# Performance work log

Hardware: AMD Instinct MI355X
Metric: run time of the kernel (lower is better)

## Reference

```python
import jax, jax.numpy as jnp
import numpy as np

N_NODES = 100000
DROPOUT_P = 0.2


def _gcn_conv(x, W, b, src, dst, n_nodes):
    # PyG GCNConv: h = x @ W; add self-loops; sym-norm deg^-1/2 aggregation; + bias
    h = x @ W  # [N, D_out]
    loops = jnp.arange(n_nodes, dtype=src.dtype)
    src_all = jnp.concatenate([src, loops])
    dst_all = jnp.concatenate([dst, loops])
    deg = jax.ops.segment_sum(jnp.ones_like(dst_all, dtype=h.dtype), dst_all,
                              num_segments=n_nodes)  # includes self-loops
    dinv = jnp.where(deg > 0, jax.lax.rsqrt(deg), 0.0)
    norm = dinv[src_all] * dinv[dst_all]  # [E+N]
    msg = h[src_all] * norm[:, None]      # gather + scale
    out = jax.ops.segment_sum(msg, dst_all, num_segments=n_nodes)  # scatter-add
    return out + b


def setup_inputs() -> dict:
    key = jax.random.key(0)
    k1, k2, k3, k4 = jax.random.split(key, 4)
    x = jax.random.normal(k1, (N_NODES, 128), dtype=jnp.float32)
    edge_index = jax.random.randint(k2, (2, 1600000), 0, N_NODES, dtype=jnp.int64)
    W1 = jax.random.normal(k3, (128, 64), dtype=jnp.float32) * (1.0 / np.sqrt(128))
    b1 = jnp.zeros((64,), dtype=jnp.float32)
    W2 = jax.random.normal(k4, (64, 32), dtype=jnp.float32) * (1.0 / np.sqrt(64))
    b2 = jnp.zeros((32,), dtype=jnp.float32)
    return {"x": x, "edge_index": edge_index, "W1": W1, "b1": b1, "W2": W2, "b2": b2}


def reference(x, edge_index, W1, b1, W2, b2):
    src, dst = edge_index[0], edge_index[1]
    h1 = _gcn_conv(x, W1, b1, src, dst, N_NODES)
    h1 = jax.nn.relu(h1)
    # F.dropout defaults to training=True -> apply inverted dropout with fixed key
    keep = jax.random.bernoulli(jax.random.key(42), 1.0 - DROPOUT_P, h1.shape)
    h1 = jnp.where(keep, h1 / (1.0 - DROPOUT_P), 0.0)
    h2 = _gcn_conv(h1, W2, b2, src, dst, N_NODES)
    return h2
```

## Files before the change

### kernel.cpp

```cpp
#include <hip/hip_runtime.h>
#include <stdint.h>

#define DIN 128
#define D1 64
#define D2 32
#define MAXDEG 48
#define BCAP 4608
#define BINBLK 4096
#define NBKPAD 512

__device__ __forceinline__ unsigned short f2bf(float v) {
  unsigned u = __float_as_uint(v);
  unsigned r = u + 0x7fffu + ((u >> 16) & 1u);
  return (unsigned short)(r >> 16);
}
__device__ __forceinline__ float bflo(unsigned u) { return __uint_as_float(u << 16); }
__device__ __forceinline__ float bfhi(unsigned u) { return __uint_as_float(u & 0xffff0000u); }

__device__ __forceinline__ unsigned rotl32(unsigned x, int r) {
  return (x << r) | (x >> (32 - r));
}

__device__ __forceinline__ unsigned threefry_fold(unsigned ctr) {
  unsigned k0 = 0u, k1 = 42u;
  unsigned ks0 = k0, ks1 = k1, ks2 = k0 ^ k1 ^ 0x1BD11BDAu;
  unsigned x0 = 0u, x1 = ctr;
  x0 += ks0; x1 += ks1;
#define TF_ROUND(r) { x0 += x1; x1 = rotl32(x1, (r)); x1 ^= x0; }
  TF_ROUND(13) TF_ROUND(15) TF_ROUND(26) TF_ROUND(6)
  x0 += ks1; x1 += ks2 + 1u;
  TF_ROUND(17) TF_ROUND(29) TF_ROUND(16) TF_ROUND(24)
  x0 += ks2; x1 += ks0 + 2u;
  TF_ROUND(13) TF_ROUND(15) TF_ROUND(26) TF_ROUND(6)
  x0 += ks0; x1 += ks1 + 3u;
  TF_ROUND(17) TF_ROUND(29) TF_ROUND(16) TF_ROUND(24)
  x0 += ks1; x1 += ks2 + 4u;
  TF_ROUND(13) TF_ROUND(15) TF_ROUND(26) TF_ROUND(6)
  x0 += ks2; x1 += ks0 + 5u;
#undef TF_ROUND
  return x0 ^ x1;
}

__device__ __forceinline__ float dropout_scale(unsigned idx) {
  unsigned bits = threefry_fold(idx);
  float u = __uint_as_float((bits >> 9) | 0x3f800000u) - 1.0f;
  return (u < 0.8f) ? 1.25f : 0.0f;
}

__device__ __forceinline__ uint4 grow64(const unsigned short* p, int s, int fc) {
  return *(const uint4*)((const char*)p + (((unsigned)s << 7) + ((unsigned)fc << 1)));
}
__device__ __forceinline__ uint4 grow32(const unsigned short* p, int s, int fc) {
  return *(const uint4*)((const char*)p + (((unsigned)s << 6) + ((unsigned)fc << 1)));
}

__device__ __forceinline__ void addpk(float2& a, unsigned u) {
  a.x += bflo(u);
  a.y += bfhi(u);
}
__device__ __forceinline__ void addpkm(float2& a, unsigned u, float m) {
  a.x = fmaf(m, bflo(u), a.x);
  a.y = fmaf(m, bfhi(u), a.y);
}

template <int K>
__device__ __forceinline__ void gather_acc1(float2 (&acc)[4], int sv, float dvv, int cnt,
                                            int d, int fc,
                                            const unsigned short* __restrict__ h1p, int eslot) {
  uint4 v[K];
  float dv[K];
#pragma unroll
  for (int seg = 0; seg < K - 1; seg++) {
    int e = seg * 8 + eslot;
    int s = __shfl(sv, e, 64);
    dv[seg] = __shfl(dvv, e, 64);
    v[seg] = grow64(h1p, s, fc);
  }
  {
    const int elast = (K - 1) * 8 + eslot;
    const bool ok = elast < cnt;
    int s = __shfl(sv, elast, 64);
    float dl = __shfl(dvv, elast, 64);
    dv[K - 1] = ok ? dl : 0.0f;
    v[K - 1] = grow64(h1p, ok ? s : d, fc);
  }
#pragma unroll
  for (int seg = 0; seg < K; seg++) {
    addpkm(acc[0], v[seg].x, dv[seg]); addpkm(acc[1], v[seg].y, dv[seg]);
    addpkm(acc[2], v[seg].z, dv[seg]); addpkm(acc[3], v[seg].w, dv[seg]);
  }
}

template <int K>
__device__ __forceinline__ void gather_acc2(float2 (&acc)[4], int sv, int cnt, int d, int fc,
                                            const unsigned short* __restrict__ h2p, int eslot) {
  uint4 v[K];
#pragma unroll
  for (int seg = 0; seg < K - 1; seg++) {
    int s = __shfl(sv, seg * 16 + eslot, 64);
    v[seg] = grow32(h2p, s, fc);
  }
  const int elast = (K - 1) * 16 + eslot;
  const bool ok = elast < cnt;
  {
    int s = __shfl(sv, elast, 64);
    v[K - 1] = grow32(h2p, ok ? s : d, fc);
  }
#pragma unroll
  for (int seg = 0; seg < K - 1; seg++) {
    addpk(acc[0], v[seg].x); addpk(acc[1], v[seg].y);
    addpk(acc[2], v[seg].z); addpk(acc[3], v[seg].w);
  }
  const float m = ok ? 1.0f : 0.0f;
  addpkm(acc[0], v[K - 1].x, m); addpkm(acc[1], v[K - 1].y, m);
  addpkm(acc[2], v[K - 1].z, m); addpkm(acc[3], v[K - 1].w, m);
}

struct BinShared {
  int cnt[NBKPAD];
  int cbase[NBKPAD];
};
struct G1Shared {
  float xT[32][65];
  float Wl[32][D1];
};
union K1Shared {
  BinShared bin;
  G1Shared g1;
};

__global__ __launch_bounds__(256) void fused1_kernel(const int* __restrict__ src,
                                                     const int* __restrict__ dst,
                                                     int* __restrict__ cursor,
                                                     unsigned* __restrict__ binned,
                                                     int E, int NBK, int nbin,
                                                     const float* __restrict__ x,
                                                     const float* __restrict__ W1,
                                                     unsigned short* __restrict__ h1p, int N) {
  __shared__ K1Shared sh;
  const int tid = threadIdx.x;

  if ((int)blockIdx.x < nbin) {
    const int e0 = blockIdx.x * BINBLK;
    const bool full = (e0 + BINBLK) <= E;

    for (int b = tid; b < NBKPAD; b += 256) sh.bin.cnt[b] = 0;
    __syncthreads();

    int dreg[16];
    if (full) {
#pragma unroll
      for (int i = 0; i < 4; i++) {
        int4 q = *(const int4*)(dst + e0 + 4 * tid + 1024 * i);
        dreg[4 * i + 0] = q.x; dreg[4 * i + 1] = q.y;
        dreg[4 * i + 2] = q.z; dreg[4 * i + 3] = q.w;
      }
    } else {
#pragma unroll
      for (int i = 0; i < 16; i++) {
        int e = e0 + 4 * tid + 1024 * (i >> 2) + (i & 3);
        dreg[i] = (e < E) ? dst[e] : -1;
      }
    }
#pragma unroll
    for (int i = 0; i < 16; i++)
      if (dreg[i] >= 0) atomicAdd(&sh.bin.cnt[dreg[i] >> 8], 1);
    __syncthreads();

    for (int b = tid; b < NBK; b += 256) {
      int c = sh.bin.cnt[b];
      if (c > 0) sh.bin.cbase[b] = b * BCAP + atomicAdd(&cursor[b], c);
      sh.bin.cnt[b] = 0;
    }
    __syncthreads();

    int sreg[16];
    if (full) {
#pragma unroll
      for (int i = 0; i < 4; i++) {
        int4 q = *(const int4*)(src + e0 + 4 * tid + 1024 * i);
        sreg[4 * i + 0] = q.x; sreg[4 * i + 1] = q.y;
        sreg[4 * i + 2] = q.z; sreg[4 * i + 3] = q.w;
      }
    } else {
#pragma unroll
      for (int i = 0; i < 16; i++) {
        int e = e0 + 4 * tid + 1024 * (i >> 2) + (i & 3);
        sreg[i] = (e < E) ? src[e] : 0;
      }
    }
#pragma unroll
    for (int i = 0; i < 16; i++) {
      int d = dreg[i];
      if (d >= 0) {
        int b = d >> 8;
        int rk = atomicAdd(&sh.bin.cnt[b], 1);
        int pos = sh.bin.cbase[b] + rk;
        if (pos - b * BCAP < BCAP)
          binned[pos] = ((unsigned)(d & 255) << 24) | (unsigned)sreg[i];
      }
    }
  } else {
    const int rowbase = ((int)blockIdx.x - nbin) * 64;
    const int tx = tid & 15;
    const int ty = tid >> 4;
    float acc[4][4];
#pragma unroll
    for (int i = 0; i < 4; i++)
#pragma unroll
      for (int j = 0; j < 4; j++) acc[i][j] = 0.f;

    for (int c4 = 0; c4 < 4; c4++) {
      const int k0 = c4 * 32;
#pragma unroll
      for (int i = 0; i < 2; i++) {
        int f = tid + 256 * i;
        int row = f >> 3;
        int kq = (f & 7) * 4;
        int gr = rowbase + row;
        float4 vv = make_float4(0.f, 0.f, 0.f, 0.f);
        if (gr < N) vv = *(const float4*)(x + (size_t)gr * DIN + k0 + kq);
        sh.g1.xT[kq + 0][row] = vv.x;
        sh.g1.xT[kq + 1][row] = vv.y;
        sh.g1.xT[kq + 2][row] = vv.z;
        sh.g1.xT[kq + 3][row] = vv.w;
      }
#pragma unroll
      for (int i = 0; i < 2; i++) {
        int f = tid + 256 * i;
        int k = f >> 4;
        int cc = (f & 15) * 4;
        *(float4*)&sh.g1.Wl[k][cc] = *(const float4*)(W1 + (size_t)(k0 + k) * D1 + cc);
      }
      __syncthreads();
#pragma unroll 4
      for (int k = 0; k < 32; k++) {
        float4 a = *(const float4*)&sh.g1.xT[k][4 * ty];
        float4 b = *(const float4*)&sh.g1.Wl[k][4 * tx];
        float av[4] = {a.x, a.y, a.z, a.w};
        float bv[4] = {b.x, b.y, b.z, b.w};
#pragma unroll
        for (int i = 0; i < 4; i++)
#pragma unroll
          for (int j = 0; j < 4; j++) acc[i][j] = fmaf(av[i], bv[j], acc[i][j]);
      }
      __syncthreads();
    }

#pragma unroll
    for (int i = 0; i < 4; i++) {
      int gr = rowbase + 4 * ty + i;
      if (gr < N) {
        ushort4 o;
        o.x = f2bf(acc[i][0]);
        o.y = f2bf(acc[i][1]);
        o.z = f2bf(acc[i][2]);
        o.w = f2bf(acc[i][3]);
        *(ushort4*)(h1p + (size_t)gr * D1 + 4 * tx) = o;
      }
    }
  }
}

__global__ __launch_bounds__(256) void ellbuild_kernel(const unsigned* __restrict__ binned,
                                                       const int* __restrict__ cursor,
                                                       int* __restrict__ deg,
                                                       float* __restrict__ dinv,
                                                       int* __restrict__ ell, int N) {
  __shared__ int r[256];
  __shared__ int ellw[256 * MAXDEG];
  const int tid = threadIdx.x;
  const int b = blockIdx.x;
  const int nodebase = b << 8;
  r[tid] = 0;
  __syncthreads();

  int cnt = cursor[b];
  if (cnt > BCAP) cnt = BCAP;
  const unsigned* seg = binned + (size_t)b * BCAP;
  for (int i = tid; i < cnt; i += 256) {
    unsigned p = seg[i];
    int local = (int)(p >> 24);
    int rk = atomicAdd(&r[local], 1);
    if (rk < MAXDEG) ellw[local * MAXDEG + rk] = (int)(p & 0x00FFFFFFu);
  }
  __syncthreads();

  int4* dst4 = (int4*)(ell + (size_t)nodebase * MAXDEG);
  const int4* src4 = (const int4*)ellw;
#pragma unroll
  for (int i = 0; i < (256 * MAXDEG / 4) / 256; i++)
    dst4[tid + 256 * i] = src4[tid + 256 * i];

  int node = nodebase + tid;
  if (node < N) {
    int dg = r[tid];
    deg[node] = dg;
    dinv[node] = (float)(1.0 / sqrt((double)(dg + 1)));
  }
}

__global__ __launch_bounds__(256) void agg1_kernel(const int* __restrict__ deg,
                                                   const float* __restrict__ dinv,
                                                   const int* __restrict__ ell,
                                                   const unsigned short* __restrict__ h1p,
                                                   const float* __restrict__ b1,
                                                   const float* __restrict__ W2,
                                                   unsigned short* __restrict__ h2p, int N) {
  __shared__ float red[4][528];
  __shared__ float W2l[D1 * D2];
  const int tid = threadIdx.x;
  const int wslot = __builtin_amdgcn_readfirstlane(tid >> 6);
  const int d = blockIdx.x * 4 + wslot;
  const int lane = tid & 63;
  const int eslot = lane >> 3;
  const int fc = (lane & 7) << 3;
  const int f = fc + eslot;
  const int c = lane & 31;
  const int h = lane >> 5;
  const int cnt = min(deg[d], MAXDEG);
  const int base = d * MAXDEG;

  {
    float4* w4 = (float4*)W2l;
    const float4* g4 = (const float4*)W2;
    w4[tid] = g4[tid];
    w4[tid + 256] = g4[tid + 256];
  }

  int sv = ell[base + lane];
  sv = (lane < cnt) ? sv : d;
  float dvv = dinv[sv];
  uint4 self = grow64(h1p, d, fc);
  const float di = dinv[d];
  const float bias = b1[f];
  const float drop = dropout_scale((unsigned)(d * D1 + f));

  __syncthreads();

  float2 acc[4];
  {
    float m = (eslot == 0) ? di : 0.0f;
    acc[0] = make_float2(m * bflo(self.x), m * bfhi(self.x));
    acc[1] = make_float2(m * bflo(self.y), m * bfhi(self.y));
    acc[2] = make_float2(m * bflo(self.z), m * bfhi(self.z));
    acc[3] = make_float2(m * bflo(self.w), m * bfhi(self.w));
  }

  switch ((cnt + 7) >> 3) {
    case 6: gather_acc1<6>(acc, sv, dvv, cnt, d, fc, h1p, eslot); break;
    case 5: gather_acc1<5>(acc, sv, dvv, cnt, d, fc, h1p, eslot); break;
    case 4: gather_acc1<4>(acc, sv, dvv, cnt, d, fc, h1p, eslot); break;
    case 3: gather_acc1<3>(acc, sv, dvv, cnt, d, fc, h1p, eslot); break;
    case 2: gather_acc1<2>(acc, sv, dvv, cnt, d, fc, h1p, eslot); break;
    case 1: gather_acc1<1>(acc, sv, dvv, cnt, d, fc, h1p, eslot); break;
    default: break;
  }

  float* wred = red[wslot];
  *(float4*)&wred[eslot * 66 + fc]     = make_float4(acc[0].x, acc[0].y, acc[1].x, acc[1].y);
  *(float4*)&wred[eslot * 66 + fc + 4] = make_float4(acc[2].x, acc[2].y, acc[3].x, acc[3].y);
  float vsum = 0.f;
#pragma unroll
  for (int e = 0; e < 8; e++) vsum += wred[e * 66 + f];

  float o = fmaf(di, vsum, bias);
  o = fmaxf(o, 0.0f);
  o *= drop;

  wred[f] = o;
  const float* w2h = &W2l[(h * 32) * D2 + c];
  float p = 0.f;
#pragma unroll
  for (int i = 0; i < 8; i++) {
    float4 hv = *(const float4*)&wred[h * 32 + 4 * i];
    p = fmaf(hv.x, w2h[(4 * i + 0) * D2], p);
    p = fmaf(hv.y, w2h[(4 * i + 1) * D2], p);
    p = fmaf(hv.z, w2h[(4 * i + 2) * D2], p);
    p = fmaf(hv.w, w2h[(4 * i + 3) * D2], p);
  }
  p += __shfl_down(p, 32, 64);
  if (h == 0) h2p[(size_t)d * D2 + c] = f2bf(di * p);
}

__global__ __launch_bounds__(256) void agg2_kernel(const int* __restrict__ deg,
                                                   const float* __restrict__ dinv,
                                                   const int* __restrict__ ell,
                                                   const unsigned short* __restrict__ h2p,
                                                   const float* __restrict__ b2,
                                                   float* __restrict__ out, int N) {
  __shared__ float red[4][544];
  const int wslot = __builtin_amdgcn_readfirstlane(threadIdx.x >> 6);
  const int d = blockIdx.x * 4 + wslot;
  const int lane = threadIdx.x & 63;
  const int eslot = lane >> 2;
  const int fc = (lane & 3) << 3;
  const int cnt = min(deg[d], MAXDEG);
  const int base = d * MAXDEG;

  int sv = ell[base + lane];
  uint4 self = grow32(h2p, d, fc);
  const float di = dinv[d];

  float2 acc[4];
  {
    float m = (eslot == 0) ? 1.0f : 0.0f;
    acc[0] = make_float2(m * bflo(self.x), m * bfhi(self.x));
    acc[1] = make_float2(m * bflo(self.y), m * bfhi(self.y));
    acc[2] = make_float2(m * bflo(self.z), m * bfhi(self.z));
    acc[3] = make_float2(m * bflo(self.w), m * bfhi(self.w));
  }

  switch ((cnt + 15) >> 4) {
    case 3: gather_acc2<3>(acc, sv, cnt, d, fc, h2p, eslot); break;
    case 2: gather_acc2<2>(acc, sv, cnt, d, fc, h2p, eslot); break;
    case 1: gather_acc2<1>(acc, sv, cnt, d, fc, h2p, eslot); break;
    default: break;
  }

  float* wred = red[wslot];
  *(float4*)&wred[eslot * 34 + fc]     = make_float4(acc[0].x, acc[0].y, acc[1].x, acc[1].y);
  *(float4*)&wred[eslot * 34 + fc + 4] = make_float4(acc[2].x, acc[2].y, acc[3].x, acc[3].y);
  const int f = fc + (eslot & 7);
  const int ebase = (lane >= 32) ? 8 : 0;
  float vsum = 0.f;
#pragma unroll
  for (int e = 0; e < 8; e++) vsum += wred[(ebase + e) * 34 + f];
  vsum += __shfl_down(vsum, 32, 64);

  if (lane < 32) {
    out[(size_t)d * D2 + f] = fmaf(di, vsum, b2[f]);
  }
}

extern "C" void kernel_launch(void* const* d_in, const int* in_sizes, int n_in,
                              void* d_out, int out_size, void* d_ws, size_t ws_size,
                              hipStream_t stream) {
  const float* x  = (const float*)d_in[0];
  const int*   ei = (const int*)d_in[1];
  const float* W1 = (const float*)d_in[2];
  const float* b1 = (const float*)d_in[3];
  const float* W2 = (const float*)d_in[4];
  const float* b2 = (const float*)d_in[5];
  const int N = in_sizes[0] / DIN;
  const int E = in_sizes[1] / 2;
  const int NBK = (N + 255) >> 8;
  const int* src = ei;
  const int* dst = ei + E;
  float* out = (float*)d_out;

  char* ws = (char*)d_ws;
  size_t off = 0;
  auto alloc = [&](size_t bytes) -> char* {
    char* p = ws + off;
    off += (bytes + 255) / 256 * 256;
    return p;
  };
  unsigned short* h1p = (unsigned short*)alloc((size_t)N * D1 * 2);
  unsigned short* h2p = (unsigned short*)alloc((size_t)N * D2 * 2);
  char*       scratch = alloc((size_t)NBK * BCAP * 4);
  int*            ell = (int*)alloc(((size_t)NBK * 256 * MAXDEG + 64) * 4);
  int*            deg = (int*)alloc((size_t)N * 4);
  float*        dinvp = (float*)alloc((size_t)N * 4);
  int*         cursor = (int*)alloc((size_t)NBK * 4);
  unsigned*    binned = (unsigned*)scratch;
  (void)ws_size; (void)n_in; (void)out_size;

  hipMemsetAsync(cursor, 0, (size_t)NBK * 4, stream);

  const int NB_BIN = (E + BINBLK - 1) / BINBLK;
  const int NB_G1 = (N + 63) / 64;
  fused1_kernel<<<NB_BIN + NB_G1, 256, 0, stream>>>(src, dst, cursor, binned, E, NBK, NB_BIN,
                                                    x, W1, h1p, N);
  ellbuild_kernel<<<NBK, 256, 0, stream>>>(binned, cursor, deg, dinvp, ell, N);
  agg1_kernel<<<N / 4, 256, 0, stream>>>(deg, dinvp, ell, h1p, b1, W2, h2p, N);
  agg2_kernel<<<N / 4, 256, 0, stream>>>(deg, dinvp, ell, h2p, b2, out, N);
}
```

Baseline: 248.6 us.

## Stage binned edges in shared memory and flush contiguous per-bucket runs

```diff
diff --git a/kernel.cpp b/kernel.cpp
--- a/kernel.cpp
+++ b/kernel.cpp
@@ -118,7 +118,9 @@
 
 struct BinShared {
   int cnt[NBKPAD];
-  int cbase[NBKPAD];
+  int cnt2[NBKPAD];
+  int gdelta[NBKPAD];
+  unsigned pairbuf[BINBLK];
 };
 struct G1Shared {
   float xT[32][65];
@@ -144,7 +146,7 @@
     const int e0 = blockIdx.x * BINBLK;
     const bool full = (e0 + BINBLK) <= E;
 
-    for (int b = tid; b < NBKPAD; b += 256) sh.bin.cnt[b] = 0;
+    for (int b = tid; b < NBKPAD; b += 256) { sh.bin.cnt[b] = 0; sh.bin.cnt2[b] = 0; }
     __syncthreads();
 
     int dreg[16];
@@ -167,11 +169,30 @@
       if (dreg[i] >= 0) atomicAdd(&sh.bin.cnt[dreg[i] >> 8], 1);
     __syncthreads();
 
-    for (int b = tid; b < NBK; b += 256) {
-      int c = sh.bin.cnt[b];
-      if (c > 0) sh.bin.cbase[b] = b * BCAP + atomicAdd(&cursor[b], c);
-      sh.bin.cnt[b] = 0;
-    }
+    int c0 = sh.bin.cnt[tid], c1 = sh.bin.cnt[tid + 256];
+    for (int off = 1; off < NBKPAD; off <<= 1) {
+      int a0 = sh.bin.cnt[tid];
+      int a1 = sh.bin.cnt[tid + 256];
+      int b0 = (tid >= off) ? sh.bin.cnt[tid - off] : 0;
+      int b1 = (tid + 256 >= off) ? sh.bin.cnt[tid + 256 - off] : 0;
+      __syncthreads();
+      sh.bin.cnt[tid] = a0 + b0;
+      sh.bin.cnt[tid + 256] = a1 + b1;
+      __syncthreads();
+    }
+    int lb0 = sh.bin.cnt[tid] - c0;
+    int lb1 = sh.bin.cnt[tid + 256] - c1;
+    if (tid < NBK && c0 > 0) {
+      int g = tid * BCAP + atomicAdd(&cursor[tid], c0);
+      sh.bin.gdelta[tid] = g - lb0;
+    }
+    if (tid + 256 < NBK && c1 > 0) {
+      int g = (tid + 256) * BCAP + atomicAdd(&cursor[tid + 256], c1);
+      sh.bin.gdelta[tid + 256] = g - lb1;
+    }
+    __syncthreads();
+    sh.bin.cnt[tid] = lb0;
+    sh.bin.cnt[tid + 256] = lb1;
     __syncthreads();
 
     int sreg[16];
@@ -194,10 +215,23 @@
       int d = dreg[i];
       if (d >= 0) {
         int b = d >> 8;
-        int rk = atomicAdd(&sh.bin.cnt[b], 1);
-        int pos = sh.bin.cbase[b] + rk;
-        if (pos - b * BCAP < BCAP)
-          binned[pos] = ((unsigned)(d & 255) << 24) | (unsigned)sreg[i];
+        int r = atomicAdd(&sh.bin.cnt2[b], 1);
+        sh.bin.pairbuf[sh.bin.cnt[b] + r] =
+            ((unsigned)(d & 255) << 24) | (unsigned)sreg[i];
+      }
+    }
+    __syncthreads();
+
+    const int lane = tid & 63;
+    const int wv = tid >> 6;
+    for (int b = wv; b < NBK; b += 4) {
+      int lb = sh.bin.cnt[b];
+      int c = sh.bin.cnt2[b];
+      int gd = (c > 0) ? sh.bin.gdelta[b] : 0;
+      for (int i = lane; i < c; i += 64) {
+        int gpos = gd + lb + i;
+        if (gpos - b * BCAP < BCAP)
+          binned[gpos] = sh.bin.pairbuf[lb + i];
       }
     }
   } else {
```

Measured after the change: 245.2 us. Within noise of the previous version (-1.4%).
